# Optimization experiments

Measured on AMD Instinct MI355X. Metric: run time of the kernel, lower is better.

Reference implementation:

```python
import jax, jax.numpy as jnp
import numpy as np

HEADS = 8
DIM_HEAD = 64
CHUNK = 128
EPS = 1e-6
KERNEL_EPS = 1e-4


def softmax_kernel(x, proj, is_query):
    # x: [b,h,n,d], proj: [f,d]  (FAVOR+ positive softmax features)
    d = x.shape[-1]
    data_normalizer = d ** -0.25
    ratio = proj.shape[0] ** -0.5
    data_dash = jnp.einsum('bhnd,fd->bhnf', x * data_normalizer, proj)
    diag = 0.5 * (data_normalizer ** 2) * jnp.sum(x * x, axis=-1, keepdims=True)  # [b,h,n,1]
    if is_query:
        m = jnp.max(data_dash, axis=-1, keepdims=True)
    else:
        m = jnp.max(data_dash, axis=(-1, -2), keepdims=True)
    return ratio * (jnp.exp(data_dash - diag - jax.lax.stop_gradient(m)) + KERNEL_EPS)


def infer_hidden_states(q, k, v, chunk_size=CHUNK):
    # q,k: [b,h,n,f], v: [b,h,n,e]; chunked causal linear attention with carried cumsums
    b, h, n, f = q.shape
    e = v.shape[-1]
    nc = n // chunk_size

    def to_chunks(t):
        return jnp.moveaxis(t.reshape(b, h, nc, chunk_size, t.shape[-1]), 2, 0)

    qs, ks, vs = to_chunks(q), to_chunks(k), to_chunks(v)

    def step(carry, inp):
        Z, S = carry  # [b,h,1,f], [b,h,1,f,e]
        qc, kc, vc = inp
        k_cum = Z + jnp.cumsum(kc, axis=2)                       # [b,h,c,f]
        D_inv = 1.0 / jnp.einsum('bhnf,bhnf->bhn', qc, k_cum + EPS)
        ctx = jnp.einsum('bhnf,bhne->bhnfe', kc, vc)             # [b,h,c,f,e]
        ctx_cum = S + jnp.cumsum(ctx, axis=2)
        out = jnp.einsum('bhnfe,bhnf,bhn->bhne', ctx_cum, qc, D_inv)
        return (k_cum[:, :, -1:], ctx_cum[:, :, -1:]), out

    init = (jnp.zeros((b, h, 1, f), q.dtype), jnp.zeros((b, h, 1, f, e), q.dtype))
    (Z, S), outs = jax.lax.scan(step, init, (qs, ks, vs))
    out = jnp.moveaxis(outs, 0, 2).reshape(b, h, n, e)
    return out, Z[:, :, 0], S[:, :, 0]


def reference(x, proj, Wq, Wk, Wv, Wo, bo):
    b, n, dim = x.shape
    h, dh = HEADS, DIM_HEAD

    def split_heads(t):
        return jnp.transpose(t.reshape(b, n, h, dh), (0, 2, 1, 3))

    q = split_heads(x @ Wq)
    k = split_heads(x @ Wk)
    v = split_heads(x @ Wv)

    qf = softmax_kernel(q, proj, is_query=True)
    kf = softmax_kernel(k, proj, is_query=False)

    out, Z, S = infer_hidden_states(qf, kf, v)
    out = jnp.transpose(out, (0, 2, 1, 3)).reshape(b, n, h * dh)
    out = out @ Wo + bo
    return out, Z, S


def setup_inputs() -> dict:
    key = jax.random.key(0)
    ks = jax.random.split(key, 6)
    b, n, dim = 2, 2048, 512
    f = 256
    return {
        'x': jax.random.normal(ks[0], (b, n, dim), jnp.float32),
        'proj': jax.random.normal(ks[1], (f, DIM_HEAD), jnp.float32),
        'Wq': jax.random.normal(ks[2], (dim, dim), jnp.float32) * (dim ** -0.5),
        'Wk': jax.random.normal(ks[3], (dim, dim), jnp.float32) * (dim ** -0.5),
        'Wv': jax.random.normal(ks[4], (dim, dim), jnp.float32) * (dim ** -0.5),
        'Wo': jax.random.normal(ks[5], (dim, dim), jnp.float32) * (dim ** -0.5),
        'bo': jnp.zeros((dim,), jnp.float32),
    }
```

## Files before the change

### kernel.cpp

```cpp
#include <hip/hip_runtime.h>
#include <hip/hip_bf16.h>
#include <math.h>

#define NB    2
#define NSEQ  2048
#define DIMM  512
#define NH    8
#define DHd   64
#define FF    256
#define CHK   128
#define NCHK  16
#define NBH   16

typedef unsigned short ushort_t;
typedef __attribute__((ext_vector_type(8))) __bf16 bf16x8;
typedef __attribute__((ext_vector_type(4))) float floatx4;

__device__ __forceinline__ unsigned short f2bf(float x) {
    union { __hip_bfloat16 h; unsigned short u; } v;
    v.h = __float2bfloat16(x);
    return v.u;
}
__device__ __forceinline__ float bf2f(unsigned short u) {
    union { unsigned short u2[2]; float f; } v;
    v.u2[0] = 0; v.u2[1] = u;
    return v.f;
}
__device__ __forceinline__ unsigned enc_f(float x) {
    unsigned u = __float_as_uint(x);
    return (u & 0x80000000u) ? ~u : (u | 0x80000000u);
}
__device__ __forceinline__ float dec_f(unsigned e) {
    unsigned u = (e & 0x80000000u) ? (e & 0x7fffffffu) : ~e;
    return __uint_as_float(u);
}

__device__ __forceinline__ void gload16(const void* g, void* l) {
    __builtin_amdgcn_global_load_lds(
        (const __attribute__((address_space(1))) void*)g,
        (__attribute__((address_space(3))) void*)l, 16, 0, 0);
}

__device__ __forceinline__ bf16x8 frag8(const ushort_t* lds, int row, int kb) {
    return *((const bf16x8*)lds + row * 8 + (kb ^ (row & 7)));
}
__device__ __forceinline__ bf16x8 fragS(const ushort_t* lds, int row, int kb) {
    return *((const bf16x8*)lds + row * 16 + (kb ^ (row & 15)));
}

__device__ __forceinline__ void stage8(const ushort_t* __restrict__ G, ushort_t* dst,
                                       int ld, int tid) {
#pragma unroll
    for (int t = 0; t < 4; t++) {
        const int g = t * 256 + tid, r = g >> 3, kb = (g & 7) ^ (r & 7);
        gload16(G + (size_t)r * ld + kb * 8, dst + (size_t)g * 8);
    }
}
__device__ __forceinline__ void stage4h(const ushort_t* __restrict__ G, ushort_t* dst,
                                        int ld, int tid) {
#pragma unroll
    for (int t = 0; t < 2; t++) {
        const int g = t * 256 + tid, r = g >> 3, kb = (g & 7) ^ (r & 7);
        gload16(G + (size_t)r * ld + kb * 8, dst + (size_t)g * 8);
    }
}
__device__ __forceinline__ void stageV(const ushort_t* __restrict__ G, ushort_t* dst,
                                       int tid) {
#pragma unroll
    for (int t = 0; t < 4; t++) {
        const int g = t * 256 + tid, r = g >> 4, kb = (g & 15) ^ (r & 15);
        gload16(G + (size_t)r * NSEQ + kb * 8, dst + (size_t)g * 8);
    }
}

__global__ __launch_bounds__(256)
void prep(const float* __restrict__ x, const float* __restrict__ proj,
          const float* __restrict__ W0, const float* __restrict__ W1,
          const float* __restrict__ W2, const float* __restrict__ W3,
          ushort_t* __restrict__ xb, ushort_t* __restrict__ projb,
          ushort_t* __restrict__ T0, ushort_t* __restrict__ T1,
          ushort_t* __restrict__ T2, ushort_t* __restrict__ T3,
          unsigned* __restrict__ mk_u)
{
    __shared__ float t[32][33];
    const int b = blockIdx.x, tid = threadIdx.x;
    if (b < 2048) {
        const int gid = b * 256 + tid;
        const float4 v = *(const float4*)(x + (size_t)gid * 4);
        union { ushort4 v4; unsigned short s[4]; } pk;
        pk.s[0] = f2bf(v.x); pk.s[1] = f2bf(v.y); pk.s[2] = f2bf(v.z); pk.s[3] = f2bf(v.w);
        ((ushort4*)xb)[gid] = pk.v4;
    } else if (b < 2064) {
        const int gid = (b - 2048) * 256 + tid;
        const float dn = 0.35355339059327379f;
        const float4 v = *(const float4*)(proj + (size_t)gid * 4);
        union { ushort4 v4; unsigned short s[4]; } pk;
        pk.s[0] = f2bf(v.x * dn); pk.s[1] = f2bf(v.y * dn);
        pk.s[2] = f2bf(v.z * dn); pk.s[3] = f2bf(v.w * dn);
        ((ushort4*)projb)[gid] = pk.v4;
    } else if (b < 3088) {
        const int idx = b - 2064;
        const int z = idx >> 8, rem = idx & 255;
        const int bx = rem & 15, by = rem >> 4;
        const float* W = (z == 0) ? W0 : (z == 1) ? W1 : (z == 2) ? W2 : W3;
        ushort_t* T = (z == 0) ? T0 : (z == 1) ? T1 : (z == 2) ? T2 : T3;
        const int x0 = bx * 32, y0 = by * 32;
        const int tx = tid & 31, ty = tid >> 5;
#pragma unroll
        for (int i = 0; i < 4; i++)
            t[ty + i * 8][tx] = W[(size_t)(y0 + ty + i * 8) * DIMM + x0 + tx];
        __syncthreads();
#pragma unroll
        for (int i = 0; i < 4; i++)
            T[(size_t)(x0 + ty + i * 8) * DIMM + y0 + tx] = f2bf(t[tx][ty + i * 8]);
    } else {
        if (tid < NBH) mk_u[tid] = 0u;
    }
}

__device__ __forceinline__ void mfma_mainloop(
    const ushort_t* __restrict__ AG, const ushort_t* __restrict__ BG,
    ushort_t* As, ushort_t* Bs, int ldA, int ldB, int K,
    floatx4 acc[4][4], int tid)
{
    const int lane = tid & 63, wid = tid >> 6;
    const int q = lane >> 4, c = lane & 15;
    const int wm = (wid >> 1) * 64, wn = (wid & 1) * 64;

    for (int k0 = 0; k0 < K; k0 += 64) {
#pragma unroll
        for (int t = 0; t < 4; t++) {
            const int g = t * 256 + tid, r = g >> 3, kb = (g & 7) ^ (r & 7);
            gload16(AG + (size_t)r * ldA + k0 + kb * 8, As + (size_t)g * 8);
        }
#pragma unroll
        for (int t = 0; t < 4; t++) {
            const int g = t * 256 + tid, r = g >> 3, kb = (g & 7) ^ (r & 7);
            gload16(BG + (size_t)r * ldB + k0 + kb * 8, Bs + (size_t)g * 8);
        }
        __syncthreads();
#pragma unroll
        for (int ks = 0; ks < 2; ks++) {
            bf16x8 af[4], bfr[4];
#pragma unroll
            for (int i = 0; i < 4; i++) {
                af[i]  = frag8(As, wm + i * 16 + c, ks * 4 + q);
                bfr[i] = frag8(Bs, wn + i * 16 + c, ks * 4 + q);
            }
#pragma unroll
            for (int i = 0; i < 4; i++)
#pragma unroll
                for (int j = 0; j < 4; j++)
                    acc[i][j] = __builtin_amdgcn_mfma_f32_16x16x32_bf16(
                        af[i], bfr[j], acc[i][j], 0, 0, 0);
        }
        __syncthreads();
    }
}

__global__ __launch_bounds__(256)
void gemm_qkv(const ushort_t* __restrict__ xb,
              const ushort_t* __restrict__ Wtq, const ushort_t* __restrict__ Wtk,
              const ushort_t* __restrict__ Wtv, const ushort_t* __restrict__ projb,
              ushort_t* __restrict__ qb, ushort_t* __restrict__ kb,
              ushort_t* __restrict__ vTb, unsigned* __restrict__ mk_u)
{
    __shared__ alignas(16) ushort_t SM[25600];
    __shared__ float red[256];
    ushort_t* As = SM;
    ushort_t* Bs = SM + 8192;
    ushort_t* PS = SM + 17408;
    const int tid = threadIdx.x;
    const int bid = blockIdx.x;
    const int z = bid % 3, tt = bid / 3;
    const int n0 = (tt & 3) * 128, m0 = (tt >> 2) * 128;
    const ushort_t* Bt = (z == 0) ? Wtq : ((z == 1) ? Wtk : Wtv);

    floatx4 zero = {0.f, 0.f, 0.f, 0.f};
    floatx4 acc[4][4];
#pragma unroll
    for (int i = 0; i < 4; i++)
#pragma unroll
        for (int j = 0; j < 4; j++) acc[i][j] = zero;

    mfma_mainloop(xb + (size_t)m0 * DIMM, Bt + (size_t)n0 * DIMM, As, Bs,
                  DIMM, DIMM, DIMM, acc, tid);

    const int lane = tid & 63, wid = tid >> 6;
    const int q = lane >> 4, cl = lane & 15;
    const int wm = (wid >> 1) * 64, wn = (wid & 1) * 64;

#pragma unroll
    for (int i = 0; i < 4; i++)
#pragma unroll
        for (int j = 0; j < 4; j++) {
            const int col = wn + j * 16 + cl;
#pragma unroll
            for (int r = 0; r < 4; r++) {
                const int row = wm + i * 16 + q * 4 + r;
                SM[row * 136 + col] = f2bf(acc[i][j][r]);
            }
        }
    __syncthreads();

    if (z < 2) {
        ushort_t* ob = (z == 0) ? qb : kb;
        if (z == 1) {
#pragma unroll
            for (int t = 0; t < 4; t++) {
                const int g = t * 256 + tid, f = g >> 3, kbg = (g & 7) ^ (f & 7);
                gload16(projb + (size_t)f * 64 + kbg * 8, PS + (size_t)g * 8);
            }
        }
#pragma unroll
        for (int p = 0; p < 16; p++) {
            const int idx = p * 256 + tid;
            const int row = idx >> 5, c4 = idx & 31;
            ushort4 o = *(const ushort4*)&SM[row * 136 + c4 * 4];
            *(ushort4*)(ob + (size_t)(m0 + row) * DIMM + n0 + c4 * 4) = o;
        }
        if (z == 1) {
            const int bb = m0 >> 11;
            const int h0 = n0 >> 6;
            float mx[2] = {-3.0e38f, -3.0e38f};
#pragma unroll
            for (int half = 0; half < 2; half++) {
                __syncthreads();
#pragma unroll
                for (int hh = 0; hh < 2; hh++) {
                    floatx4 a2[4][4];
#pragma unroll
                    for (int i = 0; i < 4; i++)
#pragma unroll
                        for (int j = 0; j < 4; j++) a2[i][j] = zero;
#pragma unroll
                    for (int ks = 0; ks < 2; ks++) {
                        bf16x8 af[4], bfr[4];
#pragma unroll
                        for (int i = 0; i < 4; i++)
                            af[i] = *(const bf16x8*)&SM[(wm + i * 16 + cl) * 136 + hh * 64 + (ks * 4 + q) * 8];
#pragma unroll
                        for (int j = 0; j < 4; j++)
                            bfr[j] = frag8(PS, wn + j * 16 + cl, ks * 4 + q);
#pragma unroll
                        for (int i = 0; i < 4; i++)
#pragma unroll
                            for (int j = 0; j < 4; j++)
                                a2[i][j] = __builtin_amdgcn_mfma_f32_16x16x32_bf16(
                                    af[i], bfr[j], a2[i][j], 0, 0, 0);
                    }
#pragma unroll
                    for (int i = 0; i < 4; i++)
#pragma unroll
                        for (int j = 0; j < 4; j++)
#pragma unroll
                            for (int r = 0; r < 4; r++) mx[hh] = fmaxf(mx[hh], a2[i][j][r]);
                }
                if (half == 0) {
                    __syncthreads();
#pragma unroll
                    for (int t = 0; t < 4; t++) {
                        const int g = t * 256 + tid, f = g >> 3, kbg = (g & 7) ^ (f & 7);
                        gload16(projb + (size_t)(128 + f) * 64 + kbg * 8, PS + (size_t)g * 8);
                    }
                }
            }
#pragma unroll
            for (int hh = 0; hh < 2; hh++) {
                __syncthreads();
                red[tid] = mx[hh];
                __syncthreads();
                for (int s = 128; s > 0; s >>= 1) {
                    if (tid < s) red[tid] = fmaxf(red[tid], red[tid + s]);
                    __syncthreads();
                }
                if (tid == 0) atomicMax(&mk_u[bb * NH + h0 + hh], enc_f(red[0]));
            }
        }
    } else {
        const int bb = m0 >> 11, nbase = m0 & 2047;
#pragma unroll
        for (int p = 0; p < 16; p++) {
            const int idx = p * 256 + tid;
            const int cl2 = idx >> 5, n4 = idx & 31;
            const int C = n0 + cl2;
            const int h = C >> 6, e = C & 63;
            union { ushort4 v4; unsigned short s[4]; } pk;
#pragma unroll
            for (int k = 0; k < 4; k++) pk.s[k] = SM[(n4 * 4 + k) * 136 + cl2];
            *(ushort4*)(vTb + (((size_t)(bb * NH + h) * 64 + e)) * NSEQ + nbase + n4 * 4) = pk.v4;
        }
    }
}

__global__ __launch_bounds__(256)
void gemm_out(const ushort_t* __restrict__ attnb, const ushort_t* __restrict__ Wto,
              float* __restrict__ out, const float* __restrict__ bias)
{
    __shared__ alignas(16) ushort_t As[4096];
    __shared__ alignas(16) ushort_t Bs[8192];
    const int tid = threadIdx.x;
    const int n0 = blockIdx.x * 128, m0 = blockIdx.y * 64;
    const ushort_t* AG = attnb + (size_t)m0 * DIMM;
    const ushort_t* BG = Wto + (size_t)n0 * DIMM;

    floatx4 zero = {0.f, 0.f, 0.f, 0.f};
    floatx4 acc[2][4];
#pragma unroll
    for (int i = 0; i < 2; i++)
#pragma unroll
        for (int j = 0; j < 4; j++) acc[i][j] = zero;

    const int lane = tid & 63, wid = tid >> 6;
    const int q = lane >> 4, c = lane & 15;
    const int wm = (wid >> 1) * 32, wn = (wid & 1) * 64;

    for (int k0 = 0; k0 < DIMM; k0 += 64) {
        stage4h(AG + k0, As, DIMM, tid);
        stage8(BG + k0, Bs, DIMM, tid);
        __syncthreads();
#pragma unroll
        for (int ks = 0; ks < 2; ks++) {
            bf16x8 af[2], bfr[4];
#pragma unroll
            for (int i = 0; i < 2; i++) af[i] = frag8(As, wm + i * 16 + c, ks * 4 + q);
#pragma unroll
            for (int j = 0; j < 4; j++) bfr[j] = frag8(Bs, wn + j * 16 + c, ks * 4 + q);
#pragma unroll
            for (int i = 0; i < 2; i++)
#pragma unroll
                for (int j = 0; j < 4; j++)
                    acc[i][j] = __builtin_amdgcn_mfma_f32_16x16x32_bf16(
                        af[i], bfr[j], acc[i][j], 0, 0, 0);
        }
        __syncthreads();
    }

#pragma unroll
    for (int i = 0; i < 2; i++)
#pragma unroll
        for (int j = 0; j < 4; j++) {
            const int col = n0 + wn + j * 16 + c;
            const float bv = bias[col];
#pragma unroll
            for (int r = 0; r < 4; r++) {
                const int row = m0 + wm + i * 16 + q * 4 + r;
                out[(size_t)row * DIMM + col] = acc[i][j][r] + bv;
            }
        }
}

__global__ __launch_bounds__(256)
void featk(const ushort_t* __restrict__ kb_, const ushort_t* __restrict__ projb,
           const unsigned* __restrict__ mk_u, const ushort_t* __restrict__ vTb,
           ushort_t* __restrict__ kfb, float* __restrict__ CTXT,
           float* __restrict__ Ksum)
{
    __shared__ alignas(16) ushort_t SM[17408];
    __shared__ alignas(16) ushort_t Vs[8192];
    __shared__ float dtmp[256];
    __shared__ float diag_l[128];
    __shared__ float colp[2][128];
    ushort_t* As = SM;
    ushort_t* Bs = SM + 8192;
    const int tid = threadIdx.x, lane = tid & 63, wid = tid >> 6;
    const int q = lane >> 4, cl = lane & 15;
    const int m0 = blockIdx.x * 128, h = blockIdx.y, fh = blockIdx.z;
    const int bb = m0 >> 11, nloc = m0 & 2047;
    const int bh = bb * NH + h;
    const int cidx = nloc >> 7;
    const ushort_t* Aq = kb_ + (size_t)m0 * DIMM + h * 64;
    const ushort_t* Vg = vTb + ((size_t)bh * 64) * NSEQ + nloc;
    const ushort_t* Pj = projb + (size_t)fh * 128 * 64;

    {
        const int row = tid >> 1, half = tid & 1;
        float s = 0.f;
        const ushort_t* p = Aq + (size_t)row * DIMM + half * 32;
#pragma unroll
        for (int d = 0; d < 32; d += 4) {
            ushort4 w = *(const ushort4*)(p + d);
            float a = bf2f(w.x), b2 = bf2f(w.y), c2 = bf2f(w.z), d2 = bf2f(w.w);
            s += a * a + b2 * b2 + c2 * c2 + d2 * d2;
        }
        dtmp[tid] = s;
    }
    stage8(Aq, As, DIMM, tid);
    stage8(Pj, Bs, 64, tid);
    stageV(Vg, Vs, tid);
    __syncthreads();
    if (tid < 128) diag_l[tid] = (dtmp[2 * tid] + dtmp[2 * tid + 1]) * 0.0625f;

    floatx4 zero = {0.f, 0.f, 0.f, 0.f};
    floatx4 acc[4][4];
#pragma unroll
    for (int i = 0; i < 4; i++)
#pragma unroll
        for (int j = 0; j < 4; j++) acc[i][j] = zero;
    const int wm = (wid >> 1) * 64, wn = (wid & 1) * 64;
#pragma unroll
    for (int ks = 0; ks < 2; ks++) {
        bf16x8 af[4], bfr[4];
#pragma unroll
        for (int i = 0; i < 4; i++) af[i] = frag8(As, wm + i * 16 + cl, ks * 4 + q);
#pragma unroll
        for (int j = 0; j < 4; j++) bfr[j] = frag8(Bs, wn + j * 16 + cl, ks * 4 + q);
#pragma unroll
        for (int i = 0; i < 4; i++)
#pragma unroll
            for (int j = 0; j < 4; j++)
                acc[i][j] = __builtin_amdgcn_mfma_f32_16x16x32_bf16(
                    af[i], bfr[j], acc[i][j], 0, 0, 0);
    }
    __syncthreads();

    const float mk = dec_f(mk_u[bh]);
#pragma unroll
    for (int i = 0; i < 4; i++)
#pragma unroll
        for (int r = 0; r < 4; r++) {
            const int row = wm + i * 16 + q * 4 + r;
            const float cc = diag_l[row] + mk;
#pragma unroll
            for (int j = 0; j < 4; j++)
                acc[i][j][r] = 0.0625f * (__expf(acc[i][j][r] - cc) + 1.0e-4f);
        }

#pragma unroll
    for (int j = 0; j < 4; j++) {
        float s = 0.f;
#pragma unroll
        for (int i = 0; i < 4; i++)
            s += acc[i][j][0] + acc[i][j][1] + acc[i][j][2] + acc[i][j][3];
        s += __shfl_xor(s, 16);
        s += __shfl_xor(s, 32);
        if (q == 0) colp[wid >> 1][wn + j * 16 + cl] = s;
    }

#pragma unroll
    for (int i = 0; i < 4; i++)
#pragma unroll
        for (int j = 0; j < 4; j++) {
            const int col = wn + j * 16 + cl;
#pragma unroll
            for (int r = 0; r < 4; r++) {
                const int row = wm + i * 16 + q * 4 + r;
                SM[row * 136 + col] = f2bf(acc[i][j][r]);
            }
        }
    __syncthreads();

    if (tid < 128)
        Ksum[((size_t)bh * NCHK + cidx) * FF + fh * 128 + tid] = colp[0][tid] + colp[1][tid];

    const size_t frow = (size_t)bh * NSEQ + nloc;
#pragma unroll
    for (int p = 0; p < 16; p++) {
        const int idx = p * 256 + tid;
        const int row = idx >> 5, c4 = idx & 31;
        ushort4 o = *(const ushort4*)&SM[row * 136 + c4 * 4];
        *(ushort4*)(kfb + (frow + row) * FF + fh * 128 + c4 * 4) = o;
    }
    __syncthreads();

    ushort_t* T = SM;
    const size_t cbase = ((size_t)bh * NCHK + cidx) * 64;
#pragma unroll
    for (int fq = 0; fq < 2; fq++) {
        if ((wid & 1) == fq) {
#pragma unroll
            for (int jj = 0; jj < 4; jj++) {
#pragma unroll
                for (int i = 0; i < 4; i++)
#pragma unroll
                    for (int r = 0; r < 4; r++) {
                        const int n = wm + i * 16 + q * 4 + r;
                        T[(jj * 16 + cl) * 136 + n] = f2bf(acc[i][jj][r]);
                    }
            }
        }
        __syncthreads();
        floatx4 accc[4];
#pragma unroll
        for (int jj = 0; jj < 4; jj++) accc[jj] = zero;
#pragma unroll
        for (int kt = 0; kt < 4; kt++) {
            const bf16x8 av = fragS(Vs, wid * 16 + cl, kt * 4 + q);
#pragma unroll
            for (int jj = 0; jj < 4; jj++) {
                const bf16x8 bv = *(const bf16x8*)(T + (jj * 16 + cl) * 136 + (kt * 4 + q) * 8);
                accc[jj] = __builtin_amdgcn_mfma_f32_16x16x32_bf16(av, bv, accc[jj], 0, 0, 0);
            }
        }
#pragma unroll
        for (int jj = 0; jj < 4; jj++) {
            const int f = fh * 128 + fq * 64 + jj * 16 + cl;
#pragma unroll
            for (int r = 0; r < 4; r++) {
                const int e = wid * 16 + q * 4 + r;
                CTXT[(cbase + e) * FF + f] = accc[jj][r];
            }
        }
        __syncthreads();
    }
}

__global__ void prefix_zs(float* __restrict__ Ksum, float* __restrict__ Zout,
                          const float* __restrict__ CTXT, ushort_t* __restrict__ ctxp,
                          float* __restrict__ Sout)
{
    const int b = blockIdx.x;
    if (b < 1024) {
        const int idx = b * 256 + threadIdx.x;
        const int bh = idx >> 14, ef = idx & 16383;
        const int e = ef >> 8, f = ef & 255;
        float run = 0.f;
#pragma unroll
        for (int c = 0; c < NCHK; c++) {
            const size_t o = (((size_t)bh * NCHK + c) * 64 + e) * FF + f;
            const float t = CTXT[o];
            ctxp[o] = f2bf(run);
            run += t;
        }
        Sout[((size_t)bh * FF + f) * 64 + e] = run;
    } else {
        const int idx = (b - 1024) * 256 + threadIdx.x;
        const int bh = idx >> 8, f = idx & 255;
        float run = 0.f;
#pragma unroll
        for (int c = 0; c < NCHK; c++) {
            const size_t o = ((size_t)(bh * NCHK + c)) * FF + f;
            const float t = Ksum[o];
            Ksum[o] = run;
            run += t;
        }
        Zout[(size_t)bh * FF + f] = run;
    }
}

__device__ __forceinline__ void st1_step(const ushort_t* QFs, const ushort_t* Bk,
                                         floatx4 acc1[8], int wv, int cl, int q)
{
#pragma unroll
    for (int ks = 0; ks < 2; ks++) {
        const bf16x8 af = frag8(QFs, wv * 16 + cl, ks * 4 + q);
        bf16x8 bfr[8];
#pragma unroll
        for (int j = 0; j < 8; j++) bfr[j] = frag8(Bk, j * 16 + cl, ks * 4 + q);
#pragma unroll
        for (int j = 0; j < 8; j++)
            acc1[j] = __builtin_amdgcn_mfma_f32_16x16x32_bf16(af, bfr[j], acc1[j], 0, 0, 0);
    }
}

__device__ __forceinline__ void pv4(const ushort_t* CpB, const ushort_t* QFs,
                                    floatx4 acc2[4], int wv, int cl, int q)
{
#pragma unroll
    for (int ks = 0; ks < 2; ks++) {
        const bf16x8 bfr = frag8(QFs, wv * 16 + cl, ks * 4 + q);
#pragma unroll
        for (int i = 0; i < 4; i++) {
            const bf16x8 af = frag8(CpB, i * 16 + cl, ks * 4 + q);
            acc2[i] = __builtin_amdgcn_mfma_f32_16x16x32_bf16(af, bfr, acc2[i], 0, 0, 0);
        }
    }
}

__global__ __launch_bounds__(256)
void chunk_out_half(const ushort_t* __restrict__ qb_, const ushort_t* __restrict__ projb,
                    const ushort_t* __restrict__ kfb, const ushort_t* __restrict__ vTb,
                    const float* __restrict__ Zex, const ushort_t* __restrict__ ctxp,
                    ushort_t* __restrict__ attnb)
{
    __shared__ alignas(16) ushort_t QF[16384];
    __shared__ alignas(16) ushort_t BufA[8192];
    __shared__ alignas(16) ushort_t Ssl[8192];
    __shared__ alignas(16) ushort_t BufB[4096];
    __shared__ float zeps[256];
    __shared__ float dtmp[256];
    __shared__ float diag_l[64];
    __shared__ float rows_part[64];
    __shared__ float denp[256];
    __shared__ float den_l[64];

    const int tid = threadIdx.x, lane = tid & 63, wv = tid >> 6;
    const int q = lane >> 4, cl = lane & 15;
    const int bh = blockIdx.x >> 5, r5 = blockIdx.x & 31;
    const int c = r5 >> 1, hq = r5 & 1;
    const int bb = bh >> 3, h = bh & 7;
    const int n0 = c * CHK, q0 = n0 + hq * 64;
    const ushort_t* Kf = kfb + ((size_t)bh * NSEQ + n0) * FF;
    const ushort_t* Aq = qb_ + ((size_t)(bb * NSEQ + q0)) * DIMM + h * 64;
    const ushort_t* Vt = vTb + ((size_t)bh * 64) * NSEQ + n0;
    const ushort_t* Cp = ctxp + ((size_t)bh * NCHK + c) * 64 * FF;

    zeps[tid] = Zex[((size_t)bh * NCHK + c) * FF + tid] + 1.0e-6f;

    stage4h(Aq, BufB, DIMM, tid);
    stage8(projb, BufA, 64, tid);
    stage8(projb + 128 * 64, Ssl, 64, tid);
    {
        const int row = tid >> 2, qd = tid & 3;
        float s = 0.f;
        const ushort_t* p = Aq + (size_t)row * DIMM + qd * 16;
#pragma unroll
        for (int d = 0; d < 16; d += 4) {
            ushort4 w = *(const ushort4*)(p + d);
            float a = bf2f(w.x), b2 = bf2f(w.y), c2 = bf2f(w.z), d2 = bf2f(w.w);
            s += a * a + b2 * b2 + c2 * c2 + d2 * d2;
        }
        dtmp[tid] = s;
    }
    __syncthreads();
    if (tid < 64)
        diag_l[tid] = (dtmp[4 * tid] + dtmp[4 * tid + 1] +
                       dtmp[4 * tid + 2] + dtmp[4 * tid + 3]) * 0.0625f;

    floatx4 zero = {0.f, 0.f, 0.f, 0.f};
    floatx4 accqA[8], accqB[8];
#pragma unroll
    for (int j = 0; j < 8; j++) { accqA[j] = zero; accqB[j] = zero; }
#pragma unroll
    for (int ks = 0; ks < 2; ks++) {
        const bf16x8 af = frag8(BufB, wv * 16 + cl, ks * 4 + q);
#pragma unroll
        for (int j = 0; j < 8; j++) {
            const bf16x8 b0 = frag8(BufA, j * 16 + cl, ks * 4 + q);
            accqA[j] = __builtin_amdgcn_mfma_f32_16x16x32_bf16(af, b0, accqA[j], 0, 0, 0);
        }
#pragma unroll
        for (int j = 0; j < 8; j++) {
            const bf16x8 b1 = frag8(Ssl, j * 16 + cl, ks * 4 + q);
            accqB[j] = __builtin_amdgcn_mfma_f32_16x16x32_bf16(af, b1, accqB[j], 0, 0, 0);
        }
    }
    float rmax[4];
#pragma unroll
    for (int r = 0; r < 4; r++) {
        float m = -3.0e38f;
#pragma unroll
        for (int j = 0; j < 8; j++) m = fmaxf(m, fmaxf(accqA[j][r], accqB[j][r]));
        m = fmaxf(m, __shfl_xor(m, 1)); m = fmaxf(m, __shfl_xor(m, 2));
        m = fmaxf(m, __shfl_xor(m, 4)); m = fmaxf(m, __shfl_xor(m, 8));
        rmax[r] = m;
    }
    __syncthreads();
#pragma unroll
    for (int r = 0; r < 4; r++) {
        const int rowL = wv * 16 + q * 4 + r;
        const float cc = diag_l[rowL] + rmax[r];
#pragma unroll
        for (int j = 0; j < 8; j++) {
            {
                const int col = j * 16 + cl;
                const float v = 0.0625f * (__expf(accqA[j][r] - cc) + 1.0e-4f);
                const int s = col >> 6, fp = col & 63;
                QF[s * 4096 + (rowL * 8 + ((fp >> 3) ^ (rowL & 7))) * 8 + (fp & 7)] = f2bf(v);
            }
            {
                const int col = 128 + j * 16 + cl;
                const float v = 0.0625f * (__expf(accqB[j][r] - cc) + 1.0e-4f);
                const int s = col >> 6, fp = col & 63;
                QF[s * 4096 + (rowL * 8 + ((fp >> 3) ^ (rowL & 7))) * 8 + (fp & 7)] = f2bf(v);
            }
        }
    }
    stage8(Kf, Ssl, FF, tid);
    __syncthreads();

    floatx4 acc1[8];
#pragma unroll
    for (int j = 0; j < 8; j++) acc1[j] = zero;
    stage8(Kf + 64, BufA, FF, tid);
    st1_step(QF, Ssl, acc1, wv, cl, q);
    __syncthreads();
    stage8(Kf + 128, Ssl, FF, tid);
    st1_step(QF + 4096, BufA, acc1, wv, cl, q);
    __syncthreads();
    stage8(Kf + 192, BufA, FF, tid);
    st1_step(QF + 8192, Ssl, acc1, wv, cl, q);
    __syncthreads();
    st1_step(QF + 12288, BufA, acc1, wv, cl, q);

    const int rbase = hq * 64;
#pragma unroll
    for (int r = 0; r < 4; r++) {
        const int rowL = wv * 16 + q * 4 + r;
        const int rowG = rbase + rowL;
        float part = 0.f;
#pragma unroll
        for (int j = 0; j < 8; j++) {
            const int col = j * 16 + cl;
            const float v = (col <= rowG) ? acc1[j][r] : 0.f;
            part += v;
            Ssl[(rowL * 16 + ((col >> 3) ^ (rowL & 15))) * 8 + (col & 7)] = f2bf(v);
        }
        part += __shfl_xor(part, 1); part += __shfl_xor(part, 2);
        part += __shfl_xor(part, 4); part += __shfl_xor(part, 8);
        if (cl == 0) rows_part[rowL] = part;
    }
    __syncthreads();

    stageV(Vt, BufA, tid);
    stage4h(Cp, BufB, FF, tid);
    float dacc = 0.f;
    {
        const int drow = tid >> 2, dq = tid & 3;
        const ushort_t* QQ = QF + dq * 4096;
#pragma unroll
        for (int gi = 0; gi < 8; gi++) {
            const ushort_t* gp = QQ + ((size_t)drow * 8 + (gi ^ (drow & 7))) * 8;
            const int kbase = dq * 64 + gi * 8;
#pragma unroll
            for (int e2 = 0; e2 < 8; e2++)
                dacc = fmaf(bf2f(gp[e2]), zeps[kbase + e2], dacc);
        }
    }
    __syncthreads();

    floatx4 acc2[4];
#pragma unroll
    for (int i = 0; i < 4; i++) acc2[i] = zero;
#pragma unroll
    for (int kk = 0; kk < 4; kk++) {
        const bf16x8 bfr = fragS(Ssl, wv * 16 + cl, kk * 4 + q);
#pragma unroll
        for (int i = 0; i < 4; i++) {
            const bf16x8 af = fragS(BufA, i * 16 + cl, kk * 4 + q);
            acc2[i] = __builtin_amdgcn_mfma_f32_16x16x32_bf16(af, bfr, acc2[i], 0, 0, 0);
        }
    }
    denp[tid] = dacc;
    __syncthreads();

    stage4h(Cp + 64, BufA, FF, tid);
    stage4h(Cp + 128, BufA + 4096, FF, tid);
    pv4(BufB, QF, acc2, wv, cl, q);
    __syncthreads();
    stage4h(Cp + 192, BufB, FF, tid);
    pv4(BufA, QF + 4096, acc2, wv, cl, q);
    pv4(BufA + 4096, QF + 8192, acc2, wv, cl, q);
    if (tid < 64)
        den_l[tid] = rows_part[tid] + denp[4 * tid] + denp[4 * tid + 1] +
                     denp[4 * tid + 2] + denp[4 * tid + 3];
    __syncthreads();
    pv4(BufB, QF + 12288, acc2, wv, cl, q);

    const float dinv = 1.0f / den_l[wv * 16 + cl];
#pragma unroll
    for (int i = 0; i < 4; i++)
#pragma unroll
        for (int r = 0; r < 4; r++) {
            const int e = i * 16 + q * 4 + r;
            Ssl[(wv * 16 + cl) * 68 + e] = f2bf(acc2[i][r] * dinv);
        }
    __syncthreads();
#pragma unroll
    for (int p = 0; p < 4; p++) {
        const int idx = p * 256 + tid;
        const int row = idx >> 4, e4 = idx & 15;
        ushort4 o = *(const ushort4*)&Ssl[row * 68 + e4 * 4];
        *(ushort4*)(attnb + ((size_t)(bb * NSEQ + q0 + row)) * DIMM + h * 64 + e4 * 4) = o;
    }
}

extern "C" void kernel_launch(void* const* d_in, const int* in_sizes, int n_in,
                              void* d_out, int out_size, void* d_ws, size_t ws_size,
                              hipStream_t stream)
{
    (void)in_sizes; (void)n_in; (void)out_size; (void)ws_size;
    const float* x    = (const float*)d_in[0];
    const float* proj = (const float*)d_in[1];
    const float* Wq   = (const float*)d_in[2];
    const float* Wk   = (const float*)d_in[3];
    const float* Wv   = (const float*)d_in[4];
    const float* Wo   = (const float*)d_in[5];
    const float* bo   = (const float*)d_in[6];
    float* out = (float*)d_out;

    char* W = (char*)d_ws;
    float*    CTXT = (float*)W;              W += (size_t)16777216;
    ushort_t* kfb  = (ushort_t*)W;           W += (size_t)16777216;
    ushort_t* ctxp = (ushort_t*)W;           W += (size_t)8388608;
    ushort_t* qb   = (ushort_t*)W;           W += (size_t)4194304;
    ushort_t* kb   = (ushort_t*)W;           W += (size_t)4194304;
    ushort_t* xb   = (ushort_t*)W;           W += (size_t)4194304;
    ushort_t* vTb  = (ushort_t*)W;           W += (size_t)4194304;
    ushort_t* Wtq  = (ushort_t*)W;           W += (size_t)524288;
    ushort_t* Wtk  = (ushort_t*)W;           W += (size_t)524288;
    ushort_t* Wtv  = (ushort_t*)W;           W += (size_t)524288;
    ushort_t* Wto  = (ushort_t*)W;           W += (size_t)524288;
    ushort_t* projb = (ushort_t*)W;          W += (size_t)32768;
    float*    Ksum = (float*)W;              W += (size_t)262144;
    unsigned* mk_u = (unsigned*)W;           W += (size_t)256;

    ushort_t* attnb = xb;

    float* Zout = out + (size_t)4096 * 512;
    float* Sout = Zout + (size_t)NBH * FF;

    hipLaunchKernelGGL(prep, dim3(3089), dim3(256), 0, stream,
                       x, proj, Wq, Wk, Wv, Wo, xb, projb, Wtq, Wtk, Wtv, Wto, mk_u);
    hipLaunchKernelGGL(gemm_qkv, dim3(384), dim3(256), 0, stream,
                       xb, Wtq, Wtk, Wtv, projb, qb, kb, vTb, mk_u);
    hipLaunchKernelGGL(featk, dim3(32, 8, 2), dim3(256), 0, stream,
                       kb, projb, mk_u, vTb, kfb, CTXT, Ksum);
    hipLaunchKernelGGL(prefix_zs, dim3(1040), dim3(256), 0, stream,
                       Ksum, Zout, CTXT, ctxp, Sout);
    hipLaunchKernelGGL(chunk_out_half, dim3(512), dim3(256), 0, stream,
                       qb, projb, kfb, vTb, Ksum, ctxp, attnb);
    hipLaunchKernelGGL(gemm_out, dim3(4, 64), dim3(256), 0, stream, attnb, Wto, out, bo);
}
```

Before: 136.6 us.

## Shrink GEMM tiles for more blocks and skip masked causal work in first half-chunk

The QKV projection GEMM tile shrinks from 128x128 to 64x128, doubling its grid to 768 blocks. The output GEMM tile shrinks from 64x128 to 64x64, doubling its grid to 512 blocks. Both aim to fill more of the MI355X's compute units. In the chunk-output kernel, the first half-chunk (hq=0) now computes only the 64 causally visible key columns of the intra-chunk score matrix and uses half the K depth for the score-times-V product, skipping MFMAs that were fully masked. Smaller tiles cost more redundant global loads per output element, and the extra branches add code size and register pressure.

```diff
diff --git a/kernel.cpp b/kernel.cpp
--- a/kernel.cpp
+++ b/kernel.cpp
@@ -118,37 +118,28 @@
     }
 }
 
-__device__ __forceinline__ void mfma_mainloop(
+__device__ __forceinline__ void mfma_mainloop64(
     const ushort_t* __restrict__ AG, const ushort_t* __restrict__ BG,
     ushort_t* As, ushort_t* Bs, int ldA, int ldB, int K,
-    floatx4 acc[4][4], int tid)
+    floatx4 acc[2][4], int tid)
 {
     const int lane = tid & 63, wid = tid >> 6;
     const int q = lane >> 4, c = lane & 15;
-    const int wm = (wid >> 1) * 64, wn = (wid & 1) * 64;
+    const int wm = (wid >> 1) * 32, wn = (wid & 1) * 64;
 
     for (int k0 = 0; k0 < K; k0 += 64) {
-#pragma unroll
-        for (int t = 0; t < 4; t++) {
-            const int g = t * 256 + tid, r = g >> 3, kb = (g & 7) ^ (r & 7);
-            gload16(AG + (size_t)r * ldA + k0 + kb * 8, As + (size_t)g * 8);
-        }
-#pragma unroll
-        for (int t = 0; t < 4; t++) {
-            const int g = t * 256 + tid, r = g >> 3, kb = (g & 7) ^ (r & 7);
-            gload16(BG + (size_t)r * ldB + k0 + kb * 8, Bs + (size_t)g * 8);
-        }
+        stage4h(AG + k0, As, ldA, tid);
+        stage8(BG + k0, Bs, ldB, tid);
         __syncthreads();
 #pragma unroll
         for (int ks = 0; ks < 2; ks++) {
-            bf16x8 af[4], bfr[4];
-#pragma unroll
-            for (int i = 0; i < 4; i++) {
-                af[i]  = frag8(As, wm + i * 16 + c, ks * 4 + q);
-                bfr[i] = frag8(Bs, wn + i * 16 + c, ks * 4 + q);
-            }
-#pragma unroll
-            for (int i = 0; i < 4; i++)
+            bf16x8 af[2], bfr[4];
+#pragma unroll
+            for (int i = 0; i < 2; i++) af[i] = frag8(As, wm + i * 16 + c, ks * 4 + q);
+#pragma unroll
+            for (int j = 0; j < 4; j++) bfr[j] = frag8(Bs, wn + j * 16 + c, ks * 4 + q);
+#pragma unroll
+            for (int i = 0; i < 2; i++)
 #pragma unroll
                 for (int j = 0; j < 4; j++)
                     acc[i][j] = __builtin_amdgcn_mfma_f32_16x16x32_bf16(
@@ -165,33 +156,33 @@
               ushort_t* __restrict__ qb, ushort_t* __restrict__ kb,
               ushort_t* __restrict__ vTb, unsigned* __restrict__ mk_u)
 {
-    __shared__ alignas(16) ushort_t SM[25600];
+    __shared__ alignas(16) ushort_t SM[20480];
     __shared__ float red[256];
     ushort_t* As = SM;
-    ushort_t* Bs = SM + 8192;
-    ushort_t* PS = SM + 17408;
+    ushort_t* Bs = SM + 4096;
+    ushort_t* PS = SM + 12288;
     const int tid = threadIdx.x;
     const int bid = blockIdx.x;
     const int z = bid % 3, tt = bid / 3;
-    const int n0 = (tt & 3) * 128, m0 = (tt >> 2) * 128;
+    const int n0 = (tt & 3) * 128, m0 = (tt >> 2) * 64;
     const ushort_t* Bt = (z == 0) ? Wtq : ((z == 1) ? Wtk : Wtv);
 
     floatx4 zero = {0.f, 0.f, 0.f, 0.f};
-    floatx4 acc[4][4];
-#pragma unroll
-    for (int i = 0; i < 4; i++)
+    floatx4 acc[2][4];
+#pragma unroll
+    for (int i = 0; i < 2; i++)
 #pragma unroll
         for (int j = 0; j < 4; j++) acc[i][j] = zero;
 
-    mfma_mainloop(xb + (size_t)m0 * DIMM, Bt + (size_t)n0 * DIMM, As, Bs,
-                  DIMM, DIMM, DIMM, acc, tid);
+    mfma_mainloop64(xb + (size_t)m0 * DIMM, Bt + (size_t)n0 * DIMM, As, Bs,
+                    DIMM, DIMM, DIMM, acc, tid);
 
     const int lane = tid & 63, wid = tid >> 6;
     const int q = lane >> 4, cl = lane & 15;
-    const int wm = (wid >> 1) * 64, wn = (wid & 1) * 64;
-
-#pragma unroll
-    for (int i = 0; i < 4; i++)
+    const int wm = (wid >> 1) * 32, wn = (wid & 1) * 64;
+
+#pragma unroll
+    for (int i = 0; i < 2; i++)
 #pragma unroll
         for (int j = 0; j < 4; j++) {
             const int col = wn + j * 16 + cl;
@@ -213,7 +204,7 @@
             }
         }
 #pragma unroll
-        for (int p = 0; p < 16; p++) {
+        for (int p = 0; p < 8; p++) {
             const int idx = p * 256 + tid;
             const int row = idx >> 5, c4 = idx & 31;
             ushort4 o = *(const ushort4*)&SM[row * 136 + c4 * 4];
@@ -228,29 +219,29 @@
                 __syncthreads();
 #pragma unroll
                 for (int hh = 0; hh < 2; hh++) {
-                    floatx4 a2[4][4];
-#pragma unroll
-                    for (int i = 0; i < 4; i++)
+                    floatx4 a2[2][4];
+#pragma unroll
+                    for (int i = 0; i < 2; i++)
 #pragma unroll
                         for (int j = 0; j < 4; j++) a2[i][j] = zero;
 #pragma unroll
                     for (int ks = 0; ks < 2; ks++) {
-                        bf16x8 af[4], bfr[4];
-#pragma unroll
-                        for (int i = 0; i < 4; i++)
+                        bf16x8 af[2], bfr[4];
+#pragma unroll
+                        for (int i = 0; i < 2; i++)
                             af[i] = *(const bf16x8*)&SM[(wm + i * 16 + cl) * 136 + hh * 64 + (ks * 4 + q) * 8];
 #pragma unroll
                         for (int j = 0; j < 4; j++)
                             bfr[j] = frag8(PS, wn + j * 16 + cl, ks * 4 + q);
 #pragma unroll
-                        for (int i = 0; i < 4; i++)
+                        for (int i = 0; i < 2; i++)
 #pragma unroll
                             for (int j = 0; j < 4; j++)
                                 a2[i][j] = __builtin_amdgcn_mfma_f32_16x16x32_bf16(
                                     af[i], bfr[j], a2[i][j], 0, 0, 0);
                     }
 #pragma unroll
-                    for (int i = 0; i < 4; i++)
+                    for (int i = 0; i < 2; i++)
 #pragma unroll
                         for (int j = 0; j < 4; j++)
 #pragma unroll
@@ -280,9 +271,9 @@
     } else {
         const int bb = m0 >> 11, nbase = m0 & 2047;
 #pragma unroll
-        for (int p = 0; p < 16; p++) {
+        for (int p = 0; p < 8; p++) {
             const int idx = p * 256 + tid;
-            const int cl2 = idx >> 5, n4 = idx & 31;
+            const int cl2 = idx >> 4, n4 = idx & 15;
             const int C = n0 + cl2;
             const int h = C >> 6, e = C & 63;
             union { ushort4 v4; unsigned short s[4]; } pk;
@@ -298,38 +289,38 @@
               float* __restrict__ out, const float* __restrict__ bias)
 {
     __shared__ alignas(16) ushort_t As[4096];
-    __shared__ alignas(16) ushort_t Bs[8192];
+    __shared__ alignas(16) ushort_t Bs[4096];
     const int tid = threadIdx.x;
-    const int n0 = blockIdx.x * 128, m0 = blockIdx.y * 64;
+    const int n0 = blockIdx.x * 64, m0 = blockIdx.y * 64;
     const ushort_t* AG = attnb + (size_t)m0 * DIMM;
     const ushort_t* BG = Wto + (size_t)n0 * DIMM;
 
     floatx4 zero = {0.f, 0.f, 0.f, 0.f};
-    floatx4 acc[2][4];
+    floatx4 acc[2][2];
 #pragma unroll
     for (int i = 0; i < 2; i++)
 #pragma unroll
-        for (int j = 0; j < 4; j++) acc[i][j] = zero;
+        for (int j = 0; j < 2; j++) acc[i][j] = zero;
 
     const int lane = tid & 63, wid = tid >> 6;
     const int q = lane >> 4, c = lane & 15;
-    const int wm = (wid >> 1) * 32, wn = (wid & 1) * 64;
+    const int wm = (wid >> 1) * 32, wn = (wid & 1) * 32;
 
     for (int k0 = 0; k0 < DIMM; k0 += 64) {
         stage4h(AG + k0, As, DIMM, tid);
-        stage8(BG + k0, Bs, DIMM, tid);
+        stage4h(BG + k0, Bs, DIMM, tid);
         __syncthreads();
 #pragma unroll
         for (int ks = 0; ks < 2; ks++) {
-            bf16x8 af[2], bfr[4];
+            bf16x8 af[2], bfr[2];
 #pragma unroll
             for (int i = 0; i < 2; i++) af[i] = frag8(As, wm + i * 16 + c, ks * 4 + q);
 #pragma unroll
-            for (int j = 0; j < 4; j++) bfr[j] = frag8(Bs, wn + j * 16 + c, ks * 4 + q);
+            for (int j = 0; j < 2; j++) bfr[j] = frag8(Bs, wn + j * 16 + c, ks * 4 + q);
 #pragma unroll
             for (int i = 0; i < 2; i++)
 #pragma unroll
-                for (int j = 0; j < 4; j++)
+                for (int j = 0; j < 2; j++)
                     acc[i][j] = __builtin_amdgcn_mfma_f32_16x16x32_bf16(
                         af[i], bfr[j], acc[i][j], 0, 0, 0);
         }
@@ -339,7 +330,7 @@
 #pragma unroll
     for (int i = 0; i < 2; i++)
 #pragma unroll
-        for (int j = 0; j < 4; j++) {
+        for (int j = 0; j < 2; j++) {
             const int col = n0 + wn + j * 16 + c;
             const float bv = bias[col];
 #pragma unroll
@@ -538,17 +529,18 @@
     }
 }
 
-__device__ __forceinline__ void st1_step(const ushort_t* QFs, const ushort_t* Bk,
-                                         floatx4 acc1[8], int wv, int cl, int q)
+template<int NJ>
+__device__ __forceinline__ void st1N(const ushort_t* QFs, const ushort_t* Bk,
+                                     floatx4* acc1, int wv, int cl, int q)
 {
 #pragma unroll
     for (int ks = 0; ks < 2; ks++) {
         const bf16x8 af = frag8(QFs, wv * 16 + cl, ks * 4 + q);
-        bf16x8 bfr[8];
-#pragma unroll
-        for (int j = 0; j < 8; j++) bfr[j] = frag8(Bk, j * 16 + cl, ks * 4 + q);
-#pragma unroll
-        for (int j = 0; j < 8; j++)
+        bf16x8 bfr[NJ];
+#pragma unroll
+        for (int j = 0; j < NJ; j++) bfr[j] = frag8(Bk, j * 16 + cl, ks * 4 + q);
+#pragma unroll
+        for (int j = 0; j < NJ; j++)
             acc1[j] = __builtin_amdgcn_mfma_f32_16x16x32_bf16(af, bfr[j], acc1[j], 0, 0, 0);
     }
 }
@@ -666,43 +658,73 @@
             }
         }
     }
-    stage8(Kf, Ssl, FF, tid);
+    if (hq) stage8(Kf, Ssl, FF, tid); else stage4h(Kf, Ssl, FF, tid);
     __syncthreads();
 
     floatx4 acc1[8];
 #pragma unroll
     for (int j = 0; j < 8; j++) acc1[j] = zero;
-    stage8(Kf + 64, BufA, FF, tid);
-    st1_step(QF, Ssl, acc1, wv, cl, q);
-    __syncthreads();
-    stage8(Kf + 128, Ssl, FF, tid);
-    st1_step(QF + 4096, BufA, acc1, wv, cl, q);
-    __syncthreads();
-    stage8(Kf + 192, BufA, FF, tid);
-    st1_step(QF + 8192, Ssl, acc1, wv, cl, q);
-    __syncthreads();
-    st1_step(QF + 12288, BufA, acc1, wv, cl, q);
-
-    const int rbase = hq * 64;
-#pragma unroll
-    for (int r = 0; r < 4; r++) {
-        const int rowL = wv * 16 + q * 4 + r;
-        const int rowG = rbase + rowL;
-        float part = 0.f;
-#pragma unroll
-        for (int j = 0; j < 8; j++) {
-            const int col = j * 16 + cl;
-            const float v = (col <= rowG) ? acc1[j][r] : 0.f;
-            part += v;
-            Ssl[(rowL * 16 + ((col >> 3) ^ (rowL & 15))) * 8 + (col & 7)] = f2bf(v);
-        }
-        part += __shfl_xor(part, 1); part += __shfl_xor(part, 2);
-        part += __shfl_xor(part, 4); part += __shfl_xor(part, 8);
-        if (cl == 0) rows_part[rowL] = part;
-    }
-    __syncthreads();
-
-    stageV(Vt, BufA, tid);
+    if (hq) {
+        stage8(Kf + 64, BufA, FF, tid);
+        st1N<8>(QF, Ssl, acc1, wv, cl, q);
+        __syncthreads();
+        stage8(Kf + 128, Ssl, FF, tid);
+        st1N<8>(QF + 4096, BufA, acc1, wv, cl, q);
+        __syncthreads();
+        stage8(Kf + 192, BufA, FF, tid);
+        st1N<8>(QF + 8192, Ssl, acc1, wv, cl, q);
+        __syncthreads();
+        st1N<8>(QF + 12288, BufA, acc1, wv, cl, q);
+    } else {
+        stage4h(Kf + 64, BufA, FF, tid);
+        st1N<4>(QF, Ssl, acc1, wv, cl, q);
+        __syncthreads();
+        stage4h(Kf + 128, Ssl, FF, tid);
+        st1N<4>(QF + 4096, BufA, acc1, wv, cl, q);
+        __syncthreads();
+        stage4h(Kf + 192, BufA, FF, tid);
+        st1N<4>(QF + 8192, Ssl, acc1, wv, cl, q);
+        __syncthreads();
+        st1N<4>(QF + 12288, BufA, acc1, wv, cl, q);
+    }
+
+    if (hq) {
+#pragma unroll
+        for (int r = 0; r < 4; r++) {
+            const int rowL = wv * 16 + q * 4 + r;
+            const int rowG = 64 + rowL;
+            float part = 0.f;
+#pragma unroll
+            for (int j = 0; j < 8; j++) {
+                const int col = j * 16 + cl;
+                const float v = (col <= rowG) ? acc1[j][r] : 0.f;
+                part += v;
+                Ssl[(rowL * 16 + ((col >> 3) ^ (rowL & 15))) * 8 + (col & 7)] = f2bf(v);
+            }
+            part += __shfl_xor(part, 1); part += __shfl_xor(part, 2);
+            part += __shfl_xor(part, 4); part += __shfl_xor(part, 8);
+            if (cl == 0) rows_part[rowL] = part;
+        }
+    } else {
+#pragma unroll
+        for (int r = 0; r < 4; r++) {
+            const int rowL = wv * 16 + q * 4 + r;
+            float part = 0.f;
+#pragma unroll
+            for (int j = 0; j < 4; j++) {
+                const int col = j * 16 + cl;
+                const float v = (col <= rowL) ? acc1[j][r] : 0.f;
+                part += v;
+                Ssl[(rowL * 16 + ((col >> 3) ^ (rowL & 15))) * 8 + (col & 7)] = f2bf(v);
+            }
+            part += __shfl_xor(part, 1); part += __shfl_xor(part, 2);
+            part += __shfl_xor(part, 4); part += __shfl_xor(part, 8);
+            if (cl == 0) rows_part[rowL] = part;
+        }
+    }
+    __syncthreads();
+
+    if (hq) stageV(Vt, BufA, tid); else stage4h(Vt, BufA, NSEQ, tid);
     stage4h(Cp, BufB, FF, tid);
     float dacc = 0.f;
     {
@@ -722,13 +744,25 @@
     floatx4 acc2[4];
 #pragma unroll
     for (int i = 0; i < 4; i++) acc2[i] = zero;
-#pragma unroll
-    for (int kk = 0; kk < 4; kk++) {
-        const bf16x8 bfr = fragS(Ssl, wv * 16 + cl, kk * 4 + q);
-#pragma unroll
-        for (int i = 0; i < 4; i++) {
-            const bf16x8 af = fragS(BufA, i * 16 + cl, kk * 4 + q);
-            acc2[i] = __builtin_amdgcn_mfma_f32_16x16x32_bf16(af, bfr, acc2[i], 0, 0, 0);
+    if (hq) {
+#pragma unroll
+        for (int kk = 0; kk < 4; kk++) {
+            const bf16x8 bfr = fragS(Ssl, wv * 16 + cl, kk * 4 + q);
+#pragma unroll
+            for (int i = 0; i < 4; i++) {
+                const bf16x8 af = fragS(BufA, i * 16 + cl, kk * 4 + q);
+                acc2[i] = __builtin_amdgcn_mfma_f32_16x16x32_bf16(af, bfr, acc2[i], 0, 0, 0);
+            }
+        }
+    } else {
+#pragma unroll
+        for (int kk = 0; kk < 2; kk++) {
+            const bf16x8 bfr = fragS(Ssl, wv * 16 + cl, kk * 4 + q);
+#pragma unroll
+            for (int i = 0; i < 4; i++) {
+                const bf16x8 af = frag8(BufA, i * 16 + cl, kk * 4 + q);
+                acc2[i] = __builtin_amdgcn_mfma_f32_16x16x32_bf16(af, bfr, acc2[i], 0, 0, 0);
+            }
         }
     }
     denp[tid] = dacc;
@@ -802,7 +836,7 @@
 
     hipLaunchKernelGGL(prep, dim3(3089), dim3(256), 0, stream,
                        x, proj, Wq, Wk, Wv, Wo, xb, projb, Wtq, Wtk, Wtv, Wto, mk_u);
-    hipLaunchKernelGGL(gemm_qkv, dim3(384), dim3(256), 0, stream,
+    hipLaunchKernelGGL(gemm_qkv, dim3(768), dim3(256), 0, stream,
                        xb, Wtq, Wtk, Wtv, projb, qb, kb, vTb, mk_u);
     hipLaunchKernelGGL(featk, dim3(32, 8, 2), dim3(256), 0, stream,
                        kb, projb, mk_u, vTb, kfb, CTXT, Ksum);
@@ -810,5 +844,5 @@
                        Ksum, Zout, CTXT, ctxp, Sout);
     hipLaunchKernelGGL(chunk_out_half, dim3(512), dim3(256), 0, stream,
                        qb, projb, kfb, vTb, Ksum, ctxp, attnb);
-    hipLaunchKernelGGL(gemm_out, dim3(4, 64), dim3(256), 0, stream, attnb, Wto, out, bo);
-}
+    hipLaunchKernelGGL(gemm_out, dim3(8, 64), dim3(256), 0, stream, attnb, Wto, out, bo);
+}
```

Measured after the change: 137.9 us. About the same (+0.9%).
